# Kernel tuning notes

Measured on AMD Instinct MI355X. Metric: run time of the kernel, lower is better.

Reference implementation:

```python
import jax, jax.numpy as jnp
import numpy as np

E, H, G = 1024, 16, 1          # embed_dim, num_heads, gqa_factor
HKV = H // G                   # kv heads
D = E // H                     # head_dim
EKV = HKV * D                  # kv_embed_dim
B, TQ, TK = 4, 512, 1024
CLAMP = float(-np.log(1.0 / 0.98 - 1.0))  # neg_prob_to_phi(clamp_prob=0.98)
SCALE = float(1.0 / np.sqrt(D))           # 1/norm_fact
NEG = -1e30                                # ~ -inf in log space


def monotonic_attention(phi):
    """Log-space monotonic alignment DP over the last axis.
    phi: (N, Ti, Tj) clamped transition logits. Returns log alignment probs, same shape.
    alpha[i,0] = 0 if i==0 else -inf
    alpha[i,j] = logaddexp(alpha[i,j-1] + logsigmoid(phi[i,j-1]),      # stay at row i
                           alpha[i-1,j-1] + logsigmoid(-phi[i-1,j-1])) # advance to row i
    """
    log_p = jax.nn.log_sigmoid(phi)
    log_1mp = jax.nn.log_sigmoid(-phi)
    N, Ti, Tj = phi.shape
    alpha0 = jnp.full((N, Ti), NEG, phi.dtype).at[:, 0].set(0.0)
    neg_col = jnp.full((N, 1), NEG, phi.dtype)

    def step(alpha, cols):
        lp, l1mp = cols  # each (N, Ti)
        stay = alpha + lp
        move = jnp.concatenate([neg_col, (alpha + l1mp)[:, :-1]], axis=1)
        new = jnp.logaddexp(stay, move)
        return new, new

    xs = (jnp.moveaxis(log_p[:, :, :-1], -1, 0), jnp.moveaxis(log_1mp[:, :, :-1], -1, 0))
    _, rest = jax.lax.scan(step, alpha0, xs)             # (Tj-1, N, Ti)
    alphas = jnp.concatenate([alpha0[None], rest], axis=0)  # (Tj, N, Ti)
    return jnp.moveaxis(alphas, 0, -1)                   # (N, Ti, Tj)


def setup_inputs() -> dict:
    k = jax.random.key(0)
    ks = jax.random.split(k, 5)
    bw = float(np.sqrt(6.0 / ((2 * E + 2 * EKV) + E)))  # xavier_uniform bound
    bo = float(1.0 / np.sqrt(E))                        # nn.Linear default bound
    return {
        "query": jax.random.normal(ks[0], (B, TQ, E), jnp.float32),
        "key": jax.random.normal(ks[1], (B, TK, E), jnp.float32),
        "value": jax.random.normal(ks[2], (B, TK, E), jnp.float32),
        "in_proj_weight": jax.random.uniform(ks[3], (2 * E + 2 * EKV, E), jnp.float32, -bw, bw),
        "in_proj_bias": jnp.zeros((2 * E + 2 * EKV,), jnp.float32),
        "out_w": jax.random.uniform(ks[4], (E, E), jnp.float32, -bo, bo),
        "out_b": jnp.zeros((E,), jnp.float32),
    }


def reference(query, key, value, in_proj_weight, in_proj_bias, out_w, out_b):
    qwa, qw, kw, vw = jnp.split(in_proj_weight, [E, 2 * E, 2 * E + EKV], axis=0)
    qba, qb, kb, vb = jnp.split(in_proj_bias, [E, 2 * E, 2 * E + EKV])

    def proj(x, w, b, g):
        y = x @ w.T + b
        Bx, T, _ = x.shape
        return y.reshape(Bx, T, g, HKV, D).transpose(0, 2, 3, 1, 4)  # (B,g,HKV,T,D)

    xqa = proj(query, qwa, qba, G)  # monotonic query
    xq = proj(query, qw, qb, G)     # regular query
    xk = proj(key, kw, kb, 1)
    xv = proj(value, vw, vb, 1)

    # mode = 'many_keys_one_query': DP grid has key rows, query cols
    phi = jnp.einsum('bghqc,bghkc->bghkq', xqa, xk)
    phi = jnp.tanh(phi) * CLAMP  # soft clamp
    mono = monotonic_attention(phi.reshape(-1, TK, TQ)).reshape(B, G, HKV, TK, TQ)
    mono = jnp.swapaxes(mono, -2, -1)  # (B,G,H,TQ,TK)

    reg = jnp.einsum('bghqc,bghkc->bghqk', xq, xk) * SCALE
    attn = jax.nn.softmax(reg + mono, axis=-1)
    xo = jnp.einsum('bghqk,bghkc->bghqc', attn, xv)
    xo = xo.transpose(0, 3, 1, 2, 4).reshape(B, TQ, E)
    return xo @ out_w.T + out_b
```

## Files before the change

kernel.cpp:

```cpp
#include <hip/hip_runtime.h>
#include <hip/hip_fp16.h>
#include <hip/hip_bf16.h>
#include <math.h>

typedef unsigned short u16;
typedef __attribute__((ext_vector_type(8))) short bf16x8;
typedef __attribute__((ext_vector_type(8))) unsigned short u16x8;
typedef __attribute__((ext_vector_type(4))) unsigned short u16x4;
typedef __attribute__((ext_vector_type(4))) float f32x4;

static constexpr float CLAMPF = 3.8918202981106265f;
static constexpr float SCALEF = 0.125f;
static constexpr float ASCALE = 16384.f;

__device__ __forceinline__ u16 f2bf(float x) {
    __hip_bfloat16 h = __float2bfloat16(x);
    return *reinterpret_cast<u16*>(&h);
}

__global__ __launch_bounds__(256)
void cvt_all_k(const float* __restrict__ q, const float* __restrict__ key,
               const float* __restrict__ val, const float* __restrict__ W,
               const float* __restrict__ ow,
               u16* __restrict__ QBF, u16* __restrict__ KBF,
               u16* __restrict__ VBF, u16* __restrict__ WBF,
               u16* __restrict__ OWBF)
{
    long i = (long)blockIdx.x * 256 + threadIdx.x;
    float4 v;
    u16* dst; long off;
    if (i < 524288) {
        dst = QBF; off = i;
        v = ((const float4*)q)[i];
    } else if (i < 1048576) {
        off = i - 524288;
        long r = off >> 8, c4 = off & 255;
        long b = r >> 9, tok = r & 511;
        dst = KBF;
        v = ((const float4*)key)[(b * 1024 + tok) * 256 + c4];
    } else if (i < 1572864) {
        off = i - 1048576;
        long r = off >> 8, c4 = off & 255;
        long b = r >> 9, tok = r & 511;
        dst = VBF;
        v = ((const float4*)val)[(b * 1024 + tok) * 256 + c4];
    } else if (i < 2621440) {
        dst = WBF; off = i - 1572864;
        v = ((const float4*)W)[off];
    } else if (i < 2883584) {
        dst = OWBF; off = i - 2621440;
        v = ((const float4*)ow)[off];
    } else return;
    u16x4 o; o.x = f2bf(v.x); o.y = f2bf(v.y); o.z = f2bf(v.z); o.w = f2bf(v.w);
    ((u16x4*)dst)[off] = o;
}

template<int TM, int TN, int EPI, bool TRI>
__device__ __forceinline__
void mfma_body(u16* As, u16* Bs, int bx, int by, int bz,
               const u16* __restrict__ Ag, const u16* __restrict__ Bg,
               void* __restrict__ Cg, const float* __restrict__ bias,
               int K, int lda, int ldb, int ldc,
               long sAb, long sAh, long sBb, long sBh, long sCb, long sCh,
               int hdiv)
{
    int b = bz / hdiv, h = bz % hdiv;
    const u16* A = Ag + (long)b * sAb + (long)h * sAh;
    const u16* B = Bg + (long)b * sBb + (long)h * sBh;

    int tid = threadIdx.x;
    int bm = by * TM, bn = bx * TN;

    constexpr int AC = TM / 32;
    constexpr int BC = TN / 32;
    int srow = tid >> 3;
    int scol = (tid & 7) * 8;

    int wid = tid >> 6, lane = tid & 63;
    int wr = wid >> 1, wc = wid & 1;
    constexpr int MI = TM / 32;
    constexpr int NI = TN / 32;
    int arow0 = wr * (TM / 2) + (lane & 15);
    int bcol0 = wc * (TN / 2) + (lane & 15);
    int koff = (lane >> 4) * 8;

    if constexpr (TRI) {
        if (bx > by) return;
    }

    f32x4 acc[MI][NI];
#pragma unroll
    for (int i = 0; i < MI; ++i)
#pragma unroll
        for (int j = 0; j < NI; ++j) acc[i][j] = (f32x4){0.f, 0.f, 0.f, 0.f};

    for (int kt = 0; kt < K; kt += 64) {
        u16x8 av[AC], bv[BC];
#pragma unroll
        for (int c = 0; c < AC; ++c)
            av[c] = *(const u16x8*)(A + (long)(bm + srow + 32 * c) * lda + kt + scol);
#pragma unroll
        for (int c = 0; c < BC; ++c)
            bv[c] = *(const u16x8*)(B + (long)(bn + srow + 32 * c) * ldb + kt + scol);
        __syncthreads();
#pragma unroll
        for (int c = 0; c < AC; ++c)
            *(u16x8*)&As[(srow + 32 * c) * 64 + scol] = av[c];
#pragma unroll
        for (int c = 0; c < BC; ++c)
            *(u16x8*)&Bs[(srow + 32 * c) * 64 + scol] = bv[c];
        __syncthreads();

#pragma unroll
        for (int ks = 0; ks < 2; ++ks) {
            bf16x8 af[MI], bfr[NI];
#pragma unroll
            for (int mi = 0; mi < MI; ++mi)
                af[mi] = *(const bf16x8*)&As[(arow0 + 16 * mi) * 64 + ks * 32 + koff];
#pragma unroll
            for (int ni = 0; ni < NI; ++ni)
                bfr[ni] = *(const bf16x8*)&Bs[(bcol0 + 16 * ni) * 64 + ks * 32 + koff];
#pragma unroll
            for (int mi = 0; mi < MI; ++mi)
#pragma unroll
                for (int ni = 0; ni < NI; ++ni)
                    acc[mi][ni] = __builtin_amdgcn_mfma_f32_16x16x32_bf16(
                        af[mi], bfr[ni], acc[mi][ni], 0, 0, 0);
        }
    }

    int rbase = bm + wr * (TM / 2) + (lane >> 4) * 4;
    int cbase = bn + wc * (TN / 2) + (lane & 15);
#pragma unroll
    for (int mi = 0; mi < MI; ++mi) {
#pragma unroll
        for (int ni = 0; ni < NI; ++ni) {
            int m0 = rbase + 16 * mi;
            int n = cbase + 16 * ni;
            if constexpr (EPI == 0) {
                u16* C = (u16*)Cg + (long)b * sCb + (long)h * sCh;
                float bvv = bias ? bias[n] : 0.f;
#pragma unroll
                for (int r = 0; r < 4; ++r)
                    C[(long)(m0 + r) * ldc + n] = f2bf(acc[mi][ni][r] + bvv);
            } else if constexpr (EPI == 1) {
                __half* C = (__half*)Cg + (long)b * sCb + (long)h * sCh;
#pragma unroll
                for (int r = 0; r < 4; ++r) {
                    float x = acc[mi][ni][r];
                    float e2 = __expf(2.f * x);
                    float tv = CLAMPF - (2.f * CLAMPF) * __builtin_amdgcn_rcpf(e2 + 1.f);
                    float pv = __builtin_amdgcn_rcpf(1.f + __expf(-tv));
                    C[(long)(m0 + r) * ldc + n] = __float2half(pv);
                }
            } else if constexpr (EPI == 3) {
                float* C = (float*)Cg + (long)b * sCb + (long)h * sCh;
                float bvv = bias[n];
#pragma unroll
                for (int r = 0; r < 4; ++r)
                    C[(long)(m0 + r) * ldc + n] = acc[mi][ni][r] + bvv;
            } else {
                u16* C = (u16*)Cg;
                float bvv = bias[n];
                long vaddr = ((long)(b * 16 + (n >> 6)) * 64 + (n & 63)) * 512 + m0;
                u16x4 pk;
                pk.x = f2bf(acc[mi][ni][0] + bvv);
                pk.y = f2bf(acc[mi][ni][1] + bvv);
                pk.z = f2bf(acc[mi][ni][2] + bvv);
                pk.w = f2bf(acc[mi][ni][3] + bvv);
                *(u16x4*)(C + vaddr) = pk;
            }
        }
    }
}

template<int TM, int TN, int EPI, bool TRI = false>
__global__ __launch_bounds__(256)
void mfma_nt(const u16* __restrict__ Ag, const u16* __restrict__ Bg,
             void* __restrict__ Cg, const float* __restrict__ bias,
             int K, int lda, int ldb, int ldc,
             long sAb, long sAh, long sBb, long sBh, long sCb, long sCh,
             int hdiv)
{
    __shared__ u16 As[TM * 64];
    __shared__ u16 Bs[TN * 64];
    mfma_body<TM, TN, EPI, TRI>(As, Bs, blockIdx.x, blockIdx.y, blockIdx.z,
                                Ag, Bg, Cg, bias, K, lda, ldb, ldc,
                                sAb, sAh, sBb, sBh, sCb, sCh, hdiv);
}

__global__ __launch_bounds__(256)
void proj_qk_k(const u16* __restrict__ QBF, const u16* __restrict__ KBF,
               const u16* __restrict__ WBF, const float* __restrict__ ipb,
               u16* __restrict__ XQAQ, u16* __restrict__ XK)
{
    __shared__ u16 As[128 * 64];
    __shared__ u16 Bs[128 * 64];
    int bid = blockIdx.x;
    if (bid < 128) {
        mfma_body<128, 128, 0, false>(As, Bs, bid & 7, bid >> 3, 0,
            QBF, WBF, XQAQ, ipb, 1024, 1024, 1024, 2048, 0, 0, 0, 0, 0, 0, 1);
    } else {
        int idx = bid - 128;
        mfma_body<128, 128, 0, false>(As, Bs, idx & 7, (idx >> 3) & 3, idx >> 5,
            KBF, WBF + 2097152, XK, ipb + 2048, 1024, 1024, 1024, 1024,
            524288L, 0, 0, 0, 524288L, 0, 1);
    }
}

#define DPL8(J) (*(const uint4*)(p + (long)min((J), 510) * 512 + k0))

#define DSTEP(PC, J) do { \
    const __half2* hp = (const __half2*)&(PC); \
    float pv[8]; \
    { float2 q01 = __half22float2(hp[0]); pv[0] = q01.x; pv[1] = q01.y; } \
    { float2 q23 = __half22float2(hp[1]); pv[2] = q23.x; pv[3] = q23.y; } \
    { float2 q45 = __half22float2(hp[2]); pv[4] = q45.x; pv[5] = q45.y; } \
    { float2 q67 = __half22float2(hp[3]); pv[6] = q67.x; pv[7] = q67.y; } \
    float c[8]; \
    _Pragma("unroll") \
    for (int r = 0; r < 8; ++r) c[r] = fmaf(-a[r], pv[r], a[r]); \
    float cp = __shfl_up(c[7], 1, 64); \
    if (lane == 0) cp = 0.f; \
    a[0] = fmaf(a[0], pv[0], cp); \
    _Pragma("unroll") \
    for (int r = 1; r < 8; ++r) a[r] = fmaf(a[r], pv[r], c[r - 1]); \
    uint4 st; \
    { __half2 h0 = __floats2half2_rn(a[0], a[1]), h1 = __floats2half2_rn(a[2], a[3]); \
      st.x = *(unsigned*)&h0; st.y = *(unsigned*)&h1; } \
    { __half2 h2 = __floats2half2_rn(a[4], a[5]), h3 = __floats2half2_rn(a[6], a[7]); \
      st.z = *(unsigned*)&h2; st.w = *(unsigned*)&h3; } \
    *(uint4*)(al + (long)(J) * 512 + k0) = st; \
} while (0)

__global__ __launch_bounds__(256)
void dp_v_k(const __half* __restrict__ P, __half* __restrict__ AL,
            const u16* __restrict__ QBF, const u16* __restrict__ VBF,
            const u16* __restrict__ WBF, const float* __restrict__ ipb,
            u16* __restrict__ XQAQ, u16* __restrict__ VT)
{
    __shared__ u16 As[128 * 64];
    __shared__ u16 Bs[128 * 64];
    int bid = blockIdx.x;

    if (bid >= 192) {
        int idx = bid - 192;
        mfma_body<128, 128, 0, false>(As, Bs, 8 + (idx & 7), idx >> 3, 0,
            QBF, WBF, XQAQ, ipb, 1024, 1024, 1024, 2048, 0, 0, 0, 0, 0, 0, 1);
        return;
    }
    if (bid >= 64) {
        int idx = bid - 64;
        mfma_body<128, 128, 4, false>(As, Bs, idx & 7, (idx >> 3) & 3, idx >> 5,
            VBF, WBF + 3145728, VT, ipb + 3072, 1024, 1024, 1024, 0,
            524288L, 0, 0, 0, 0, 0, 1);
        return;
    }

    if (threadIdx.x >= 64) return;
    int n = bid;
    int lane = threadIdx.x;
    const __half* p = P + (long)n * 262144;
    __half* al = AL + (long)n * 262144;
    int k0 = lane * 8;

    float a[8];
#pragma unroll
    for (int r = 0; r < 8; ++r) a[r] = 0.f;
    if (lane == 0) a[0] = ASCALE;
    {
        uint4 st;
        __half2 h0 = __floats2half2_rn(a[0], a[1]), h1 = __floats2half2_rn(a[2], a[3]);
        __half2 h2 = __floats2half2_rn(a[4], a[5]), h3 = __floats2half2_rn(a[6], a[7]);
        st.x = *(unsigned*)&h0; st.y = *(unsigned*)&h1;
        st.z = *(unsigned*)&h2; st.w = *(unsigned*)&h3;
        *(uint4*)(al + k0) = st;
    }

    int j = 1;
    uint4 f0 = DPL8(0), f1 = DPL8(1), f2 = DPL8(2), f3 = DPL8(3);
    uint4 f4 = DPL8(4), f5 = DPL8(5), f6 = DPL8(6), f7 = DPL8(7);

    while (j + 7 < 512) {
        DSTEP(f0, j); f0 = DPL8(j + 7); ++j;
        DSTEP(f1, j); f1 = DPL8(j + 7); ++j;
        DSTEP(f2, j); f2 = DPL8(j + 7); ++j;
        DSTEP(f3, j); f3 = DPL8(j + 7); ++j;
        DSTEP(f4, j); f4 = DPL8(j + 7); ++j;
        DSTEP(f5, j); f5 = DPL8(j + 7); ++j;
        DSTEP(f6, j); f6 = DPL8(j + 7); ++j;
        DSTEP(f7, j); f7 = DPL8(j + 7); ++j;
    }
    while (j < 512) {
        DSTEP(f0, j);
        f0 = f1; f1 = f2; f2 = f3; f3 = f4; f4 = f5; f5 = f6; f6 = f7;
        ++j;
    }
}

__global__ __launch_bounds__(256, 4)
void fused_attn_k(const u16* __restrict__ XQAQ, const u16* __restrict__ XK,
                  const u16* __restrict__ VT, const __half* __restrict__ AL,
                  u16* __restrict__ XO)
{
    __shared__ u16 wtile[4][2048];
    __shared__ float co[4][16][64];
    __shared__ float cml[4][2][16];

    int n = blockIdx.x; int b = n >> 4, h = n & 15;
    int tid = threadIdx.x, wave = tid >> 6, lane = tid & 63;
    int l15 = lane & 15, l4 = lane >> 4;
    int qg = blockIdx.y * 16;
    u16* wlds = wtile[wave];
    int swz = (l15 & 7) << 3;

    float m = -3.0e38f, lsum = 0.f;
    f32x4 o[4];
#pragma unroll
    for (int df = 0; df < 4; ++df) o[df] = (f32x4){0.f, 0.f, 0.f, 0.f};

    if (wave * 128 < qg + 16) {
        const u16* qbase = XQAQ + (long)(b * 512 + qg + l15) * 2048 + 1024 + h * 64 + l4 * 8;
        bf16x8 qf0 = *(const bf16x8*)(qbase);
        bf16x8 qf1 = *(const bf16x8*)(qbase + 32);

        const u16* kbase = XK + (long)(b * 512 + wave * 128 + l15) * 1024 + h * 64 + l4 * 8;
        const __half* abase = AL + (long)(n * 512 + qg + l15) * 512 + wave * 128 + l4 * 4;
        const u16* vbase = VT + (long)(n * 64 + l15) * 512 + wave * 128 + l4 * 8;

        uint2 areg[8];
#pragma unroll
        for (int kf = 0; kf < 8; ++kf)
            areg[kf] = *(const uint2*)(abase + kf * 16);

        f32x4 s[8];
#pragma unroll
        for (int kf = 0; kf < 8; ++kf) {
            const u16* kb = kbase + (long)(kf * 16) * 1024;
            bf16x8 k0 = *(const bf16x8*)kb;
            bf16x8 k1 = *(const bf16x8*)(kb + 32);
            f32x4 acc = (f32x4){0.f, 0.f, 0.f, 0.f};
            acc = __builtin_amdgcn_mfma_f32_16x16x32_bf16(k0, qf0, acc, 0, 0, 0);
            acc = __builtin_amdgcn_mfma_f32_16x16x32_bf16(k1, qf1, acc, 0, 0, 0);
            s[kf] = acc;
        }

        float mt = -3.0e38f;
#pragma unroll
        for (int kf = 0; kf < 8; ++kf)
            mt = fmaxf(mt, fmaxf(fmaxf(s[kf][0], s[kf][1]), fmaxf(s[kf][2], s[kf][3])));
        mt = fmaxf(mt, __shfl_xor(mt, 16, 64));
        mt = fmaxf(mt, __shfl_xor(mt, 32, 64));
        m = mt;
        float negm = -mt * SCALEF;

#pragma unroll
        for (int kf = 0; kf < 8; ++kf) {
            float2 a01 = __half22float2(*(__half2*)&areg[kf].x);
            float2 a23 = __half22float2(*(__half2*)&areg[kf].y);
            float w0 = a01.x * __expf(fmaf(s[kf][0], SCALEF, negm));
            float w1 = a01.y * __expf(fmaf(s[kf][1], SCALEF, negm));
            float w2 = a23.x * __expf(fmaf(s[kf][2], SCALEF, negm));
            float w3 = a23.y * __expf(fmaf(s[kf][3], SCALEF, negm));
            lsum += (w0 + w1) + (w2 + w3);
            u16x4 wp; wp.x = f2bf(w0); wp.y = f2bf(w1); wp.z = f2bf(w2); wp.w = f2bf(w3);
            *(u16x4*)&wlds[(l15 * 128 + kf * 16 + l4 * 4) ^ swz] = wp;
        }

#pragma unroll
        for (int ks2 = 0; ks2 < 4; ++ks2) {
            bf16x8 wf = *(const bf16x8*)&wlds[(l15 * 128 + ks2 * 32 + l4 * 8) ^ swz];
#pragma unroll
            for (int df = 0; df < 4; ++df) {
                const u16* vb = vbase + (long)(df * 16) * 512 + ks2 * 32;
                bf16x8 vf = *(const bf16x8*)vb;
                o[df] = __builtin_amdgcn_mfma_f32_16x16x32_bf16(wf, vf, o[df], 0, 0, 0);
            }
        }

        lsum += __shfl_xor(lsum, 16, 64);
        lsum += __shfl_xor(lsum, 32, 64);
    }

    if (lane < 16) { cml[wave][0][l15] = m; cml[wave][1][l15] = lsum; }
#pragma unroll
    for (int df = 0; df < 4; ++df)
#pragma unroll
        for (int r = 0; r < 4; ++r)
            co[wave][l4 * 4 + r][df * 16 + l15] = o[df][r];
    __syncthreads();

    int q = tid >> 4, d0 = (tid & 15) * 4;
    float m0 = cml[0][0][q], m1 = cml[1][0][q], m2 = cml[2][0][q], m3 = cml[3][0][q];
    float ms = fmaxf(fmaxf(m0, m1), fmaxf(m2, m3));
    float c0w = __expf((m0 - ms) * SCALEF), c1w = __expf((m1 - ms) * SCALEF);
    float c2w = __expf((m2 - ms) * SCALEF), c3w = __expf((m3 - ms) * SCALEF);
    float lt = c0w * cml[0][1][q] + c1w * cml[1][1][q]
             + c2w * cml[2][1][q] + c3w * cml[3][1][q];
    f32x4 o0 = *(const f32x4*)&co[0][q][d0];
    f32x4 o1 = *(const f32x4*)&co[1][q][d0];
    f32x4 o2 = *(const f32x4*)&co[2][q][d0];
    f32x4 o3 = *(const f32x4*)&co[3][q][d0];
    float inv = __builtin_amdgcn_rcpf(lt);
    u16x4 st;
#pragma unroll
    for (int j = 0; j < 4; ++j)
        st[j] = f2bf((c0w * o0[j] + c1w * o1[j] + c2w * o2[j] + c3w * o3[j]) * inv);
    *(u16x4*)&XO[(long)(b * 512 + qg + q) * 1024 + h * 64 + d0] = st;
}

extern "C" void kernel_launch(void* const* d_in, const int* in_sizes, int n_in,
                              void* d_out, int out_size, void* d_ws, size_t ws_size,
                              hipStream_t stream)
{
    const float* q   = (const float*)d_in[0];
    const float* key = (const float*)d_in[1];
    const float* val = (const float*)d_in[2];
    const float* W   = (const float*)d_in[3];
    const float* ipb = (const float*)d_in[4];
    const float* ow  = (const float*)d_in[5];
    const float* ob  = (const float*)d_in[6];
    float* out = (float*)d_out;
    char* w = (char*)d_ws;

    __half* PSIG  = (__half*)(w);
    __half* ALPHA = (__half*)(w + 33554432);
    u16*    XQAQ  = (u16*)(w + 67108864);
    u16*    XK    = (u16*)(w + 75497472);
    u16*    VT    = (u16*)(w + 79691776);
    u16*    XO    = (u16*)(w + 83886080);
    u16*    OWBF  = (u16*)(w + 88080384);
    u16*    KBF   = (u16*)(w + 90177536);
    u16*    VBF   = (u16*)(w + 94371840);
    u16*    WBF   = (u16*)(w + 98566144);
    u16*    QBF   = (u16*)(w + 83886080);

    dim3 blk(256);

    cvt_all_k<<<dim3(11264), blk, 0, stream>>>(
        q, key, val, W, ow, QBF, KBF, VBF, WBF, OWBF);

    proj_qk_k<<<dim3(256), blk, 0, stream>>>(QBF, KBF, WBF, ipb, XQAQ, XK);

    mfma_nt<128, 128, 1, true><<<dim3(4, 4, 64), blk, 0, stream>>>(
        XQAQ, XK, PSIG, nullptr, 64, 2048, 1024, 512,
        1048576L, 64, 524288L, 64, 4194304L, 262144L, 16);

    dp_v_k<<<dim3(320), blk, 0, stream>>>(PSIG, ALPHA, QBF, VBF, WBF, ipb, XQAQ, VT);

    fused_attn_k<<<dim3(64, 32, 1), blk, 0, stream>>>(XQAQ, XK, VT, ALPHA, XO);

    mfma_nt<128, 128, 3><<<dim3(8, 16, 1), blk, 0, stream>>>(
        XO, OWBF, out, ob, 1024, 1024, 1024, 1024, 0, 0, 0, 0, 0, 0, 1);
}
```

Before: 160.1 us.

## Fuse phi GEMM into DP kernel with per-tile flags so DP starts early

```diff
diff --git a/kernel.cpp b/kernel.cpp
--- a/kernel.cpp
+++ b/kernel.cpp
@@ -24,8 +24,9 @@
                const float* __restrict__ ow,
                u16* __restrict__ QBF, u16* __restrict__ KBF,
                u16* __restrict__ VBF, u16* __restrict__ WBF,
-               u16* __restrict__ OWBF)
-{
+               u16* __restrict__ OWBF, int* __restrict__ FLAG)
+{
+    if (blockIdx.x == 0 && threadIdx.x < 256) FLAG[threadIdx.x] = 0;
     long i = (long)blockIdx.x * 256 + threadIdx.x;
     float4 v;
     u16* dst; long off;
@@ -208,7 +209,7 @@
     }
 }
 
-#define DPL8(J) (*(const uint4*)(p + (long)min((J), 510) * 512 + k0))
+#define DPL8C(J) (*(const uint4*)(p + (long)min((J), jcap) * 512 + k0))
 
 #define DSTEP(PC, J) do { \
     const __half2* hp = (const __half2*)&(PC); \
@@ -234,26 +235,42 @@
 } while (0)
 
 __global__ __launch_bounds__(256)
-void dp_v_k(const __half* __restrict__ P, __half* __restrict__ AL,
-            const u16* __restrict__ QBF, const u16* __restrict__ VBF,
-            const u16* __restrict__ WBF, const float* __restrict__ ipb,
-            u16* __restrict__ XQAQ, u16* __restrict__ VT)
+void dp_all_k(const __half* __restrict__ P, __half* __restrict__ AL,
+              const u16* __restrict__ XQAQ, const u16* __restrict__ XK,
+              const u16* __restrict__ QBF, const u16* __restrict__ VBF,
+              const u16* __restrict__ WBF, const float* __restrict__ ipb,
+              u16* __restrict__ XQAQW, u16* __restrict__ VT,
+              __half* __restrict__ PSIG, int* __restrict__ FLAG)
 {
     __shared__ u16 As[128 * 64];
     __shared__ u16 Bs[128 * 64];
     int bid = blockIdx.x;
 
-    if (bid >= 192) {
-        int idx = bid - 192;
+    if (bid >= 1216) {
+        int idx = bid - 1216;
         mfma_body<128, 128, 0, false>(As, Bs, 8 + (idx & 7), idx >> 3, 0,
-            QBF, WBF, XQAQ, ipb, 1024, 1024, 1024, 2048, 0, 0, 0, 0, 0, 0, 1);
+            QBF, WBF, XQAQW, ipb, 1024, 1024, 1024, 2048, 0, 0, 0, 0, 0, 0, 1);
         return;
     }
-    if (bid >= 64) {
-        int idx = bid - 64;
+    if (bid >= 1088) {
+        int idx = bid - 1088;
         mfma_body<128, 128, 4, false>(As, Bs, idx & 7, (idx >> 3) & 3, idx >> 5,
             VBF, WBF + 3145728, VT, ipb + 3072, 1024, 1024, 1024, 0,
             524288L, 0, 0, 0, 0, 0, 1);
+        return;
+    }
+    if (bid >= 64) {
+        int idx = bid - 64;
+        int by = idx >> 8;
+        int n = (idx & 255) >> 2;
+        int bx = idx & 3;
+        if (bx > by) return;
+        mfma_body<128, 128, 1, false>(As, Bs, bx, by, n,
+            XQAQ, XK, PSIG, nullptr, 64, 2048, 1024, 512,
+            1048576L, 64, 524288L, 64, 4194304L, 262144L, 16);
+        __threadfence();
+        __syncthreads();
+        if (threadIdx.x == 0) atomicAdd(&FLAG[n * 4 + by], 1);
         return;
     }
 
@@ -277,24 +294,36 @@
         *(uint4*)(al + k0) = st;
     }
 
-    int j = 1;
-    uint4 f0 = DPL8(0), f1 = DPL8(1), f2 = DPL8(2), f3 = DPL8(3);
-    uint4 f4 = DPL8(4), f5 = DPL8(5), f6 = DPL8(6), f7 = DPL8(7);
-
-    while (j + 7 < 512) {
-        DSTEP(f0, j); f0 = DPL8(j + 7); ++j;
-        DSTEP(f1, j); f1 = DPL8(j + 7); ++j;
-        DSTEP(f2, j); f2 = DPL8(j + 7); ++j;
-        DSTEP(f3, j); f3 = DPL8(j + 7); ++j;
-        DSTEP(f4, j); f4 = DPL8(j + 7); ++j;
-        DSTEP(f5, j); f5 = DPL8(j + 7); ++j;
-        DSTEP(f6, j); f6 = DPL8(j + 7); ++j;
-        DSTEP(f7, j); f7 = DPL8(j + 7); ++j;
-    }
-    while (j < 512) {
-        DSTEP(f0, j);
-        f0 = f1; f1 = f2; f2 = f3; f3 = f4; f4 = f5; f5 = f6; f6 = f7;
-        ++j;
+    for (int t = 0; t < 4; ++t) {
+        while (atomicAdd(&FLAG[n * 4 + t], 0) < t + 1)
+            __builtin_amdgcn_s_sleep(16);
+        __threadfence();
+
+        int jbeg = (t == 0) ? 1 : 128 * t;
+        int jend = 128 * (t + 1);
+        int jcap = jend - 2;
+
+        uint4 f0 = DPL8C(jbeg - 1), f1 = DPL8C(jbeg + 0);
+        uint4 f2 = DPL8C(jbeg + 1), f3 = DPL8C(jbeg + 2);
+        uint4 f4 = DPL8C(jbeg + 3), f5 = DPL8C(jbeg + 4);
+        uint4 f6 = DPL8C(jbeg + 5), f7 = DPL8C(jbeg + 6);
+
+        int j = jbeg;
+        while (j + 7 < jend) {
+            DSTEP(f0, j); f0 = DPL8C(j + 7); ++j;
+            DSTEP(f1, j); f1 = DPL8C(j + 7); ++j;
+            DSTEP(f2, j); f2 = DPL8C(j + 7); ++j;
+            DSTEP(f3, j); f3 = DPL8C(j + 7); ++j;
+            DSTEP(f4, j); f4 = DPL8C(j + 7); ++j;
+            DSTEP(f5, j); f5 = DPL8C(j + 7); ++j;
+            DSTEP(f6, j); f6 = DPL8C(j + 7); ++j;
+            DSTEP(f7, j); f7 = DPL8C(j + 7); ++j;
+        }
+        while (j < jend) {
+            DSTEP(f0, j);
+            f0 = f1; f1 = f2; f2 = f3; f3 = f4; f4 = f5; f5 = f6; f6 = f7;
+            ++j;
+        }
     }
 }
 
@@ -433,20 +462,18 @@
     u16*    KBF   = (u16*)(w + 90177536);
     u16*    VBF   = (u16*)(w + 94371840);
     u16*    WBF   = (u16*)(w + 98566144);
+    int*    FLAG  = (int*)(w + 106954752);
     u16*    QBF   = (u16*)(w + 83886080);
 
     dim3 blk(256);
 
     cvt_all_k<<<dim3(11264), blk, 0, stream>>>(
-        q, key, val, W, ow, QBF, KBF, VBF, WBF, OWBF);
+        q, key, val, W, ow, QBF, KBF, VBF, WBF, OWBF, FLAG);
 
     proj_qk_k<<<dim3(256), blk, 0, stream>>>(QBF, KBF, WBF, ipb, XQAQ, XK);
 
-    mfma_nt<128, 128, 1, true><<<dim3(4, 4, 64), blk, 0, stream>>>(
-        XQAQ, XK, PSIG, nullptr, 64, 2048, 1024, 512,
-        1048576L, 64, 524288L, 64, 4194304L, 262144L, 16);
-
-    dp_v_k<<<dim3(320), blk, 0, stream>>>(PSIG, ALPHA, QBF, VBF, WBF, ipb, XQAQ, VT);
+    dp_all_k<<<dim3(1344), blk, 0, stream>>>(
+        PSIG, ALPHA, XQAQ, XK, QBF, VBF, WBF, ipb, XQAQ, VT, PSIG, FLAG);
 
     fused_attn_k<<<dim3(64, 32, 1), blk, 0, stream>>>(XQAQ, XK, VT, ALPHA, XO);
 
```

Measured after the change: 302.7 us. 89.0% more time.
